# Kernel tuning notes

Hardware: AMD Instinct MI355X
Metric: run time of the kernel (lower is better)

## Reference

```python
import jax, jax.numpy as jnp
import numpy as np

DIM = 128
POS_HID = 64
ATTN_HID = DIM * 4
K_NEIGH = 16


def _mlp2(x, w1, b1, w2, b2):
    # Linear -> ReLU -> Linear (weights stored as (in, out))
    return jax.nn.relu(x @ w1 + b1) @ w2 + b2


def setup_inputs() -> dict:
    key = jax.random.key(0)
    ks = jax.random.split(key, 12)
    B, N = 2, 512
    s = 0.05
    return {
        "x": jax.random.normal(ks[0], (B, DIM, N), jnp.float32),
        "pos": jax.random.normal(ks[1], (B, N, 3), jnp.float32),
        "w_qkv": jax.random.normal(ks[2], (DIM, 3 * DIM), jnp.float32) * s,
        "pos_w1": jax.random.normal(ks[3], (3, POS_HID), jnp.float32) * s,
        "pos_b1": jnp.zeros((POS_HID,), jnp.float32),
        "pos_w2": jax.random.normal(ks[4], (POS_HID, DIM), jnp.float32) * s,
        "pos_b2": jnp.zeros((DIM,), jnp.float32),
        "attn_w1": jax.random.normal(ks[5], (DIM, ATTN_HID), jnp.float32) * s,
        "attn_b1": jnp.zeros((ATTN_HID,), jnp.float32),
        "attn_w2": jax.random.normal(ks[6], (ATTN_HID, DIM), jnp.float32) * s,
        "attn_b2": jnp.zeros((DIM,), jnp.float32),
    }


def reference(x, pos, w_qkv, pos_w1, pos_b1, pos_w2, pos_b2,
              attn_w1, attn_b1, attn_w2, attn_b2):
    # x: (B, dim, N) -> (B, N, dim)
    xt = jnp.swapaxes(x, 1, 2)
    B, N, d = xt.shape

    qkv = xt @ w_qkv                           # (B, N, 3d), no bias
    q, k, v = jnp.split(qkv, 3, axis=-1)

    rel_pos = pos[:, :, None, :] - pos[:, None, :, :]          # (B, N, N, 3)
    rel_pos_emb = _mlp2(rel_pos, pos_w1, pos_b1, pos_w2, pos_b2)  # (B, N, N, d)
    qk_rel = q[:, :, None, :] - k[:, None, :, :]               # (B, N, N, d)

    # KNN: smallest euclidean rel distances per query point
    rel_dist = jnp.sqrt(jnp.sum(rel_pos * rel_pos, axis=-1))   # (B, N, N)
    _, idx = jax.lax.top_k(-rel_dist, K_NEIGH)                 # (B, N, K)

    idxe = idx[..., None]                                      # (B, N, K, 1)
    v_g = v[jnp.arange(B)[:, None, None], idx]                 # (B, N, K, d)
    qk_g = jnp.take_along_axis(qk_rel, idxe, axis=2)           # (B, N, K, d)
    pe_g = jnp.take_along_axis(rel_pos_emb, idxe, axis=2)      # (B, N, K, d)

    v_g = v_g + pe_g
    sim = _mlp2(qk_g + pe_g, attn_w1, attn_b1, attn_w2, attn_b2)  # (B, N, K, d)
    attn = jax.nn.softmax(sim, axis=-2)                        # softmax over neighbors
    agg = jnp.einsum('bikd,bikd->bid', attn, v_g)              # (B, N, d)
    return jnp.swapaxes(agg, 1, 2)                             # (B, d, N)
```

## Files before the change

### kernel.cpp

```cpp
#include <hip/hip_runtime.h>
#include <math.h>

#define DIM 128
#define N_PTS 512
#define K_NEIGH 16
#define POS_HID 64
#define ATTN_HID 512

typedef __attribute__((ext_vector_type(8))) short short8;
typedef __attribute__((ext_vector_type(4))) float f32x4;
typedef unsigned short us;
typedef unsigned long long ull;

__device__ __forceinline__ us f2b(float f) {
    unsigned int u = __builtin_bit_cast(unsigned int, f);
    u += 0x7fffu + ((u >> 16) & 1u);
    return (us)(u >> 16);
}

__device__ __forceinline__ ull shflx64(ull v, int m) {
    int lo = __shfl_xor((int)(unsigned int)v, m);
    int hi = __shfl_xor((int)(unsigned int)(v >> 32), m);
    return ((ull)(unsigned int)hi << 32) | (unsigned int)lo;
}

__global__ void pack_kernel(const float* __restrict__ wqkv,
                            const float* __restrict__ aw1,
                            const float* __restrict__ aw2,
                            const float* __restrict__ pw2,
                            us* __restrict__ p0, us* __restrict__ p1,
                            us* __restrict__ p2, us* __restrict__ p3) {
    int t = blockIdx.x * 256 + threadIdx.x;
    if (t < 49152) {
        int j = t & 7, l = (t >> 3) & 63, rem = t >> 9;
        int nt = rem % 24, ks = rem / 24;
        int k = ks * 32 + (l >> 4) * 8 + j, n = nt * 16 + (l & 15);
        p0[t] = f2b(wqkv[k * 384 + n]);
    } else if (t < 114688) {
        int u = t - 49152;
        int j = u & 7, l = (u >> 3) & 63, nt = (u >> 9) & 31, ks = u >> 14;
        int k = ks * 32 + (l >> 4) * 8 + j, n = nt * 16 + (l & 15);
        p1[u] = f2b(aw1[k * ATTN_HID + n]);
    } else if (t < 180224) {
        int u = t - 114688;
        int j = u & 7, l = (u >> 3) & 63, nt = (u >> 9) & 7, ch = u >> 12;
        int k = ch * 32 + (l >> 4) * 8 + j, n = nt * 16 + (l & 15);
        p2[u] = f2b(aw2[k * DIM + n]);
    } else if (t < 188416) {
        int u = t - 180224;
        int j = u & 7, l = (u >> 3) & 63, nt = (u >> 9) & 7, ks = u >> 12;
        int k = ks * 32 + (l >> 4) * 8 + j, n = nt * 16 + (l & 15);
        p3[u] = f2b(pw2[k * DIM + n]);
    }
}

__global__ __launch_bounds__(512)
void qkv_mfma_kernel(const float* __restrict__ x,
                     const us* __restrict__ p0,
                     float* __restrict__ qkv) {
    __shared__ __align__(16) us xA[16][136];
    const int tid = threadIdx.x;
    const int w = tid >> 6, lane = tid & 63, quad = lane >> 4, lq = lane & 15;
    const int n0 = blockIdx.x * 16;
    const int b = n0 >> 9, nn = n0 & (N_PTS - 1);
#pragma unroll
    for (int rr = 0; rr < 4; ++rr) {
        int id = rr * 512 + tid;
        int d = id >> 4, i = id & 15;
        xA[i][d] = f2b(x[(size_t)(b * DIM + d) * N_PTS + nn + i]);
    }
    __syncthreads();
    short8 a[4];
#pragma unroll
    for (int ks = 0; ks < 4; ++ks)
        a[ks] = *(const short8*)&xA[lq][ks * 32 + quad * 8];
#pragma unroll
    for (int i = 0; i < 3; ++i) {
        int nt = w * 3 + i;
        f32x4 acc = {0.f, 0.f, 0.f, 0.f};
#pragma unroll
        for (int ks = 0; ks < 4; ++ks) {
            const short8 bf = *(const short8*)(p0 + (size_t)((ks * 24 + nt) * 64 + lane) * 8);
            acc = __builtin_amdgcn_mfma_f32_16x16x32_bf16(a[ks], bf, acc, 0, 0, 0);
        }
#pragma unroll
        for (int r = 0; r < 4; ++r)
            qkv[(size_t)(n0 + quad * 4 + r) * 384 + nt * 16 + lq] = acc[r];
    }
}

__global__ __launch_bounds__(256, 2)
void attn_fused_kernel(const float* __restrict__ pos,
                       const float* __restrict__ qkv,
                       const float* __restrict__ pw1,
                       const float* __restrict__ pb1,
                       const float* __restrict__ pb2,
                       const us* __restrict__ p1,
                       const us* __restrict__ p2,
                       const us* __restrict__ p3,
                       const float* __restrict__ ab1,
                       float* __restrict__ out) {
    __shared__ __align__(16) us hinA[4][16][136];
    __shared__ __align__(16) us h1s[4][16][40];
    __shared__ int nbrs[4][16];
    __shared__ __align__(16) f32x4 cxch[4][4][64];

    const int tid = threadIdx.x;
    const int w = tid >> 6, lane = tid & 63, quad = lane >> 4, lq = lane & 15;
    const int pt = w >> 1, sub = w & 1;
    const int g = blockIdx.x * 2 + pt, b = g >> 9, n = g & (N_PTS - 1);
    const int ch0 = sub << 3;

    short8 b3f[2][8];
#pragma unroll
    for (int ks = 0; ks < 2; ++ks)
#pragma unroll
        for (int nt = 0; nt < 8; ++nt)
            b3f[ks][nt] = *(const short8*)(p3 + (size_t)((ks * 8 + nt) * 64 + lane) * 8);

    float w1x[2][8], w1y[2][8], w1z[2][8], w1b[2][8];
#pragma unroll
    for (int ks = 0; ks < 2; ++ks)
#pragma unroll
        for (int jj = 0; jj < 8; ++jj) {
            int c = ks * 32 + quad * 8 + jj;
            w1x[ks][jj] = pw1[c];
            w1y[ks][jj] = pw1[64 + c];
            w1z[ks][jj] = pw1[128 + c];
            w1b[ks][jj] = pb1[c];
        }

    float qvr[8], pb2r[8], ab1r[16];
#pragma unroll
    for (int nt = 0; nt < 8; ++nt) {
        qvr[nt]  = qkv[(size_t)g * 384 + nt * 16 + lq];
        pb2r[nt] = pb2[nt * 16 + lq];
    }
#pragma unroll
    for (int i = 0; i < 16; ++i) ab1r[i] = ab1[(sub * 16 + i) * 16 + lq];

    {
        const float pix = pos[g * 3 + 0], piy = pos[g * 3 + 1], piz = pos[g * 3 + 2];
        float d2[8];
#pragma unroll
        for (int rr = 0; rr < 8; ++rr) {
            int j = rr * 64 + lane;
            float dx = pix - pos[(b * N_PTS + j) * 3 + 0];
            float dy = piy - pos[(b * N_PTS + j) * 3 + 1];
            float dz = piz - pos[(b * N_PTS + j) * 3 + 2];
            d2[rr] = dx * dx + dy * dy + dz * dz;
        }
        for (int r = 0; r < K_NEIGH; ++r) {
            ull key = ~0ULL;
#pragma unroll
            for (int rr = 0; rr < 8; ++rr) {
                unsigned int fb = __builtin_bit_cast(unsigned int, d2[rr]);
                ull k2 = ((ull)fb << 32) | (unsigned int)(rr * 64 + lane);
                key = k2 < key ? k2 : key;
            }
#pragma unroll
            for (int off = 32; off > 0; off >>= 1) {
                ull o = shflx64(key, off);
                key = o < key ? o : key;
            }
            unsigned int jw = (unsigned int)key;
            if (lane == 0) nbrs[w][r] = (int)jw;
            if (lane == (int)(jw & 63)) d2[jw >> 6] = __builtin_inff();
        }
    }

    short8 pha[2];
    {
        const int jn = nbrs[w][lq];
        float rx = pos[g * 3 + 0] - pos[(b * N_PTS + jn) * 3 + 0];
        float ry = pos[g * 3 + 1] - pos[(b * N_PTS + jn) * 3 + 1];
        float rz = pos[g * 3 + 2] - pos[(b * N_PTS + jn) * 3 + 2];
#pragma unroll
        for (int ks = 0; ks < 2; ++ks) {
            short8 f;
#pragma unroll
            for (int jj = 0; jj < 8; ++jj) {
                float h = rx * w1x[ks][jj] + ry * w1y[ks][jj] + rz * w1z[ks][jj] + w1b[ks][jj];
                f[jj] = (short)f2b(fmaxf(h, 0.f));
            }
            pha[ks] = f;
        }
    }

    f32x4 pe[8];
#pragma unroll
    for (int nt = 0; nt < 8; ++nt) {
        f32x4 acc = {0.f, 0.f, 0.f, 0.f};
        acc = __builtin_amdgcn_mfma_f32_16x16x32_bf16(pha[0], b3f[0][nt], acc, 0, 0, 0);
        acc = __builtin_amdgcn_mfma_f32_16x16x32_bf16(pha[1], b3f[1][nt], acc, 0, 0, 0);
#pragma unroll
        for (int r = 0; r < 4; ++r) pe[nt][r] = acc[r] + pb2r[nt];
    }

    f32x4 vg[8];
    {
        int jr[4];
#pragma unroll
        for (int r = 0; r < 4; ++r) jr[r] = nbrs[w][quad * 4 + r];
#pragma unroll
        for (int nt = 0; nt < 8; ++nt) {
            int d = nt * 16 + lq;
#pragma unroll
            for (int r = 0; r < 4; ++r) {
                const float* kv = qkv + (size_t)(b * N_PTS + jr[r]) * 384;
                float pp = pe[nt][r];
                hinA[w][quad * 4 + r][d] = f2b(qvr[nt] - kv[128 + d] + pp);
                vg[nt][r] = kv[256 + d] + pp;
            }
        }
    }

    short8 a1f[4];
#pragma unroll
    for (int ks = 0; ks < 4; ++ks)
        a1f[ks] = *(const short8*)&hinA[w][lq][ks * 32 + quad * 8];

    f32x4 c2[8];
#pragma unroll
    for (int nt = 0; nt < 8; ++nt) c2[nt] = (f32x4){0.f, 0.f, 0.f, 0.f};

#pragma unroll
    for (int c = 0; c < 8; ++c) {
        const int ch = ch0 + c;
        short8 p1f[2][4];
#pragma unroll
        for (int t = 0; t < 2; ++t)
#pragma unroll
            for (int ks = 0; ks < 4; ++ks)
                p1f[t][ks] = *(const short8*)(p1 + (size_t)(((ks << 5) + ch * 2 + t) * 64 + lane) * 8);
#pragma unroll
        for (int t = 0; t < 2; ++t) {
            f32x4 acc = {0.f, 0.f, 0.f, 0.f};
#pragma unroll
            for (int ks = 0; ks < 4; ++ks)
                acc = __builtin_amdgcn_mfma_f32_16x16x32_bf16(a1f[ks], p1f[t][ks], acc, 0, 0, 0);
            float bias = ab1r[c * 2 + t];
#pragma unroll
            for (int r = 0; r < 4; ++r)
                h1s[w][quad * 4 + r][t * 16 + lq] = f2b(fmaxf(acc[r] + bias, 0.f));
        }
        short8 p2f[8];
#pragma unroll
        for (int nt2 = 0; nt2 < 8; ++nt2)
            p2f[nt2] = *(const short8*)(p2 + (size_t)(((ch << 3) + nt2) * 64 + lane) * 8);
        const short8 a2 = *(const short8*)&h1s[w][lq][quad * 8];
#pragma unroll
        for (int nt2 = 0; nt2 < 8; ++nt2)
            c2[nt2] = __builtin_amdgcn_mfma_f32_16x16x32_bf16(a2, p2f[nt2], c2[nt2], 0, 0, 0);
    }

#pragma unroll
    for (int i = 0; i < 4; ++i)
        cxch[w][i][lane] = c2[(sub ^ 1) * 4 + i];
    __syncthreads();

#pragma unroll
    for (int i = 0; i < 4; ++i) {
        const int nt2 = sub * 4 + i;
        f32x4 o = cxch[w ^ 1][i][lane];
        f32x4 s4 = c2[nt2];
        s4[0] += o[0]; s4[1] += o[1]; s4[2] += o[2]; s4[3] += o[3];

        float m = fmaxf(fmaxf(s4[0], s4[1]), fmaxf(s4[2], s4[3]));
        m = fmaxf(m, __shfl_xor(m, 16));
        m = fmaxf(m, __shfl_xor(m, 32));
        float e0 = __expf(s4[0] - m), e1 = __expf(s4[1] - m);
        float e2 = __expf(s4[2] - m), e3 = __expf(s4[3] - m);
        float s = e0 + e1 + e2 + e3;
        f32x4 v4 = vg[nt2];
        float a = e0 * v4[0] + e1 * v4[1] + e2 * v4[2] + e3 * v4[3];
        s += __shfl_xor(s, 16); s += __shfl_xor(s, 32);
        a += __shfl_xor(a, 16); a += __shfl_xor(a, 32);
        if (quad == 0)
            out[(size_t)(b * DIM + nt2 * 16 + lq) * N_PTS + n] = a / s;
    }
}

extern "C" void kernel_launch(void* const* d_in, const int* in_sizes, int n_in,
                              void* d_out, int out_size, void* d_ws, size_t ws_size,
                              hipStream_t stream) {
    const float* x    = (const float*)d_in[0];
    const float* pos  = (const float*)d_in[1];
    const float* wqkv = (const float*)d_in[2];
    const float* pw1  = (const float*)d_in[3];
    const float* pb1  = (const float*)d_in[4];
    const float* pw2  = (const float*)d_in[5];
    const float* pb2  = (const float*)d_in[6];
    const float* aw1  = (const float*)d_in[7];
    const float* ab1  = (const float*)d_in[8];
    const float* aw2  = (const float*)d_in[9];
    float* out = (float*)d_out;

    int B = in_sizes[0] / (DIM * N_PTS);
    int npts = B * N_PTS;

    char* ws = (char*)d_ws;
    float* qkv = (float*)ws;
    us* p0 = (us*)(ws + (size_t)npts * 384 * 4);
    us* p1 = p0 + 49152;
    us* p2 = p1 + 65536;
    us* p3 = p2 + 65536;

    pack_kernel<<<736, 256, 0, stream>>>(wqkv, aw1, aw2, pw2, p0, p1, p2, p3);
    qkv_mfma_kernel<<<npts / 16, 512, 0, stream>>>(x, p0, qkv);
    attn_fused_kernel<<<npts / 2, 256, 0, stream>>>(pos, qkv,
                                                    pw1, pb1, pb2,
                                                    p1, p2, p3, ab1, out);
}
```

Before: 111.4 us.

## Fuse weight packing into QKV kernel and split KNN/gather work across wave pairs

Merges the weight-pack kernel and the QKV MFMA kernel into one launch: extra blocks pack the attention and position weights, while QKV blocks read and convert wqkv directly from fp32 global memory instead of a pre-packed buffer. This removes one kernel launch and its serialization. In the attention kernel, only one of the two waves per point runs KNN, and each wave now computes half of the position-embedding and gather channels, with shared-memory barriers to exchange results. The cost is redundant bf16 conversion of wqkv in every QKV block, plus two extra block-wide synchronizations.

```diff
diff --git a/kernel.cpp b/kernel.cpp
--- a/kernel.cpp
+++ b/kernel.cpp
@@ -24,48 +24,46 @@
     return ((ull)(unsigned int)hi << 32) | (unsigned int)lo;
 }
 
-__global__ void pack_kernel(const float* __restrict__ wqkv,
-                            const float* __restrict__ aw1,
-                            const float* __restrict__ aw2,
-                            const float* __restrict__ pw2,
-                            us* __restrict__ p0, us* __restrict__ p1,
-                            us* __restrict__ p2, us* __restrict__ p3) {
-    int t = blockIdx.x * 256 + threadIdx.x;
-    if (t < 49152) {
-        int j = t & 7, l = (t >> 3) & 63, rem = t >> 9;
-        int nt = rem % 24, ks = rem / 24;
-        int k = ks * 32 + (l >> 4) * 8 + j, n = nt * 16 + (l & 15);
-        p0[t] = f2b(wqkv[k * 384 + n]);
-    } else if (t < 114688) {
-        int u = t - 49152;
-        int j = u & 7, l = (u >> 3) & 63, nt = (u >> 9) & 31, ks = u >> 14;
-        int k = ks * 32 + (l >> 4) * 8 + j, n = nt * 16 + (l & 15);
-        p1[u] = f2b(aw1[k * ATTN_HID + n]);
-    } else if (t < 180224) {
-        int u = t - 114688;
-        int j = u & 7, l = (u >> 3) & 63, nt = (u >> 9) & 7, ch = u >> 12;
-        int k = ch * 32 + (l >> 4) * 8 + j, n = nt * 16 + (l & 15);
-        p2[u] = f2b(aw2[k * DIM + n]);
-    } else if (t < 188416) {
-        int u = t - 180224;
-        int j = u & 7, l = (u >> 3) & 63, nt = (u >> 9) & 7, ks = u >> 12;
-        int k = ks * 32 + (l >> 4) * 8 + j, n = nt * 16 + (l & 15);
-        p3[u] = f2b(pw2[k * DIM + n]);
-    }
-}
-
-__global__ __launch_bounds__(512)
-void qkv_mfma_kernel(const float* __restrict__ x,
-                     const us* __restrict__ p0,
-                     float* __restrict__ qkv) {
+__global__ __launch_bounds__(256)
+void qkv_pack_kernel(const float* __restrict__ x,
+                     const float* __restrict__ wqkv,
+                     const float* __restrict__ aw1,
+                     const float* __restrict__ aw2,
+                     const float* __restrict__ pw2,
+                     float* __restrict__ qkv,
+                     us* __restrict__ p1, us* __restrict__ p2,
+                     us* __restrict__ p3, int npts) {
     __shared__ __align__(16) us xA[16][136];
     const int tid = threadIdx.x;
+    const int nq = npts >> 2;
+
+    if ((int)blockIdx.x >= nq) {
+        int t = ((int)blockIdx.x - nq) * 256 + tid;
+        if (t < 65536) {
+            int j = t & 7, l = (t >> 3) & 63, nt = (t >> 9) & 31, ks = t >> 14;
+            int k = ks * 32 + (l >> 4) * 8 + j, n = nt * 16 + (l & 15);
+            p1[t] = f2b(aw1[k * ATTN_HID + n]);
+        } else if (t < 131072) {
+            int u = t - 65536;
+            int j = u & 7, l = (u >> 3) & 63, nt = (u >> 9) & 7, ch = u >> 12;
+            int k = ch * 32 + (l >> 4) * 8 + j, n = nt * 16 + (l & 15);
+            p2[u] = f2b(aw2[k * DIM + n]);
+        } else if (t < 139264) {
+            int u = t - 131072;
+            int j = u & 7, l = (u >> 3) & 63, nt = (u >> 9) & 7, ks = u >> 12;
+            int k = ks * 32 + (l >> 4) * 8 + j, n = nt * 16 + (l & 15);
+            p3[u] = f2b(pw2[k * DIM + n]);
+        }
+        return;
+    }
+
     const int w = tid >> 6, lane = tid & 63, quad = lane >> 4, lq = lane & 15;
-    const int n0 = blockIdx.x * 16;
+    const int n0 = ((int)blockIdx.x >> 2) * 16;
+    const int ntb = ((int)blockIdx.x & 3) * 6;
     const int b = n0 >> 9, nn = n0 & (N_PTS - 1);
 #pragma unroll
-    for (int rr = 0; rr < 4; ++rr) {
-        int id = rr * 512 + tid;
+    for (int rr = 0; rr < 8; ++rr) {
+        int id = rr * 256 + tid;
         int d = id >> 4, i = id & 15;
         xA[i][d] = f2b(x[(size_t)(b * DIM + d) * N_PTS + nn + i]);
     }
@@ -75,17 +73,23 @@
     for (int ks = 0; ks < 4; ++ks)
         a[ks] = *(const short8*)&xA[lq][ks * 32 + quad * 8];
 #pragma unroll
-    for (int i = 0; i < 3; ++i) {
-        int nt = w * 3 + i;
-        f32x4 acc = {0.f, 0.f, 0.f, 0.f};
-#pragma unroll
-        for (int ks = 0; ks < 4; ++ks) {
-            const short8 bf = *(const short8*)(p0 + (size_t)((ks * 24 + nt) * 64 + lane) * 8);
-            acc = __builtin_amdgcn_mfma_f32_16x16x32_bf16(a[ks], bf, acc, 0, 0, 0);
-        }
-#pragma unroll
-        for (int r = 0; r < 4; ++r)
-            qkv[(size_t)(n0 + quad * 4 + r) * 384 + nt * 16 + lq] = acc[r];
+    for (int i = 0; i < 2; ++i) {
+        int nl = w + i * 4;
+        if (nl < 6) {
+            int nt = ntb + nl;
+            f32x4 acc = {0.f, 0.f, 0.f, 0.f};
+#pragma unroll
+            for (int ks = 0; ks < 4; ++ks) {
+                const float* wp = wqkv + (size_t)(ks * 32 + quad * 8) * 384 + nt * 16 + lq;
+                short8 bf;
+#pragma unroll
+                for (int j = 0; j < 8; ++j) bf[j] = (short)f2b(wp[(size_t)j * 384]);
+                acc = __builtin_amdgcn_mfma_f32_16x16x32_bf16(a[ks], bf, acc, 0, 0, 0);
+            }
+#pragma unroll
+            for (int r = 0; r < 4; ++r)
+                qkv[(size_t)(n0 + quad * 4 + r) * 384 + nt * 16 + lq] = acc[r];
+        }
     }
 }
 
@@ -100,9 +104,9 @@
                        const us* __restrict__ p3,
                        const float* __restrict__ ab1,
                        float* __restrict__ out) {
-    __shared__ __align__(16) us hinA[4][16][136];
+    __shared__ __align__(16) us hinA[2][16][136];
     __shared__ __align__(16) us h1s[4][16][40];
-    __shared__ int nbrs[4][16];
+    __shared__ int nbrs[2][16];
     __shared__ __align__(16) f32x4 cxch[4][4][64];
 
     const int tid = threadIdx.x;
@@ -111,12 +115,12 @@
     const int g = blockIdx.x * 2 + pt, b = g >> 9, n = g & (N_PTS - 1);
     const int ch0 = sub << 3;
 
-    short8 b3f[2][8];
+    short8 b3f[2][4];
 #pragma unroll
     for (int ks = 0; ks < 2; ++ks)
 #pragma unroll
-        for (int nt = 0; nt < 8; ++nt)
-            b3f[ks][nt] = *(const short8*)(p3 + (size_t)((ks * 8 + nt) * 64 + lane) * 8);
+        for (int i = 0; i < 4; ++i)
+            b3f[ks][i] = *(const short8*)(p3 + (size_t)((ks * 8 + sub * 4 + i) * 64 + lane) * 8);
 
     float w1x[2][8], w1y[2][8], w1z[2][8], w1b[2][8];
 #pragma unroll
@@ -130,16 +134,17 @@
             w1b[ks][jj] = pb1[c];
         }
 
-    float qvr[8], pb2r[8], ab1r[16];
-#pragma unroll
-    for (int nt = 0; nt < 8; ++nt) {
-        qvr[nt]  = qkv[(size_t)g * 384 + nt * 16 + lq];
-        pb2r[nt] = pb2[nt * 16 + lq];
+    float qvr[4], pb2r[4], ab1r[16];
+#pragma unroll
+    for (int i = 0; i < 4; ++i) {
+        int nt = sub * 4 + i;
+        qvr[i]  = qkv[(size_t)g * 384 + nt * 16 + lq];
+        pb2r[i] = pb2[nt * 16 + lq];
     }
 #pragma unroll
     for (int i = 0; i < 16; ++i) ab1r[i] = ab1[(sub * 16 + i) * 16 + lq];
 
-    {
+    if (sub == 0) {
         const float pix = pos[g * 3 + 0], piy = pos[g * 3 + 1], piz = pos[g * 3 + 2];
         float d2[8];
 #pragma unroll
@@ -164,14 +169,15 @@
                 key = o < key ? o : key;
             }
             unsigned int jw = (unsigned int)key;
-            if (lane == 0) nbrs[w][r] = (int)jw;
+            if (lane == 0) nbrs[pt][r] = (int)jw;
             if (lane == (int)(jw & 63)) d2[jw >> 6] = __builtin_inff();
         }
     }
+    __syncthreads();
 
     short8 pha[2];
     {
-        const int jn = nbrs[w][lq];
+        const int jn = nbrs[pt][lq];
         float rx = pos[g * 3 + 0] - pos[(b * N_PTS + jn) * 3 + 0];
         float ry = pos[g * 3 + 1] - pos[(b * N_PTS + jn) * 3 + 1];
         float rz = pos[g * 3 + 2] - pos[(b * N_PTS + jn) * 3 + 2];
@@ -187,38 +193,39 @@
         }
     }
 
-    f32x4 pe[8];
-#pragma unroll
-    for (int nt = 0; nt < 8; ++nt) {
+    f32x4 pe[4];
+#pragma unroll
+    for (int i = 0; i < 4; ++i) {
         f32x4 acc = {0.f, 0.f, 0.f, 0.f};
-        acc = __builtin_amdgcn_mfma_f32_16x16x32_bf16(pha[0], b3f[0][nt], acc, 0, 0, 0);
-        acc = __builtin_amdgcn_mfma_f32_16x16x32_bf16(pha[1], b3f[1][nt], acc, 0, 0, 0);
-#pragma unroll
-        for (int r = 0; r < 4; ++r) pe[nt][r] = acc[r] + pb2r[nt];
-    }
-
-    f32x4 vg[8];
+        acc = __builtin_amdgcn_mfma_f32_16x16x32_bf16(pha[0], b3f[0][i], acc, 0, 0, 0);
+        acc = __builtin_amdgcn_mfma_f32_16x16x32_bf16(pha[1], b3f[1][i], acc, 0, 0, 0);
+#pragma unroll
+        for (int r = 0; r < 4; ++r) pe[i][r] = acc[r] + pb2r[i];
+    }
+
+    f32x4 vg[4];
     {
         int jr[4];
 #pragma unroll
-        for (int r = 0; r < 4; ++r) jr[r] = nbrs[w][quad * 4 + r];
-#pragma unroll
-        for (int nt = 0; nt < 8; ++nt) {
-            int d = nt * 16 + lq;
+        for (int r = 0; r < 4; ++r) jr[r] = nbrs[pt][quad * 4 + r];
+#pragma unroll
+        for (int i = 0; i < 4; ++i) {
+            int d = (sub * 4 + i) * 16 + lq;
 #pragma unroll
             for (int r = 0; r < 4; ++r) {
                 const float* kv = qkv + (size_t)(b * N_PTS + jr[r]) * 384;
-                float pp = pe[nt][r];
-                hinA[w][quad * 4 + r][d] = f2b(qvr[nt] - kv[128 + d] + pp);
-                vg[nt][r] = kv[256 + d] + pp;
-            }
-        }
-    }
+                float pp = pe[i][r];
+                hinA[pt][quad * 4 + r][d] = f2b(qvr[i] - kv[128 + d] + pp);
+                vg[i][r] = kv[256 + d] + pp;
+            }
+        }
+    }
+    __syncthreads();
 
     short8 a1f[4];
 #pragma unroll
     for (int ks = 0; ks < 4; ++ks)
-        a1f[ks] = *(const short8*)&hinA[w][lq][ks * 32 + quad * 8];
+        a1f[ks] = *(const short8*)&hinA[pt][lq][ks * 32 + quad * 8];
 
     f32x4 c2[8];
 #pragma unroll
@@ -272,7 +279,7 @@
         float e0 = __expf(s4[0] - m), e1 = __expf(s4[1] - m);
         float e2 = __expf(s4[2] - m), e3 = __expf(s4[3] - m);
         float s = e0 + e1 + e2 + e3;
-        f32x4 v4 = vg[nt2];
+        f32x4 v4 = vg[i];
         float a = e0 * v4[0] + e1 * v4[1] + e2 * v4[2] + e3 * v4[3];
         s += __shfl_xor(s, 16); s += __shfl_xor(s, 32);
         a += __shfl_xor(a, 16); a += __shfl_xor(a, 32);
@@ -301,13 +308,14 @@
 
     char* ws = (char*)d_ws;
     float* qkv = (float*)ws;
-    us* p0 = (us*)(ws + (size_t)npts * 384 * 4);
-    us* p1 = p0 + 49152;
+    us* p1 = (us*)(ws + (size_t)npts * 384 * 4);
     us* p2 = p1 + 65536;
     us* p3 = p2 + 65536;
 
-    pack_kernel<<<736, 256, 0, stream>>>(wqkv, aw1, aw2, pw2, p0, p1, p2, p3);
-    qkv_mfma_kernel<<<npts / 16, 512, 0, stream>>>(x, p0, qkv);
+    int nq = npts / 4;
+    int grid = nq + (139264 + 255) / 256;
+    qkv_pack_kernel<<<grid, 256, 0, stream>>>(x, wqkv, aw1, aw2, pw2,
+                                              qkv, p1, p2, p3, npts);
     attn_fused_kernel<<<npts / 2, 256, 0, stream>>>(pos, qkv,
                                                     pw1, pb1, pb2,
                                                     p1, p2, p3, ab1, out);
```

Measured after the change: 104.5 us. 6.2% less time.
